# Kernel optimization log

Measured on AMD Instinct MI355X. Metric: run time of the kernel, lower is better.

## Reference

```python
import jax, jax.numpy as jnp
import numpy as np

B, T, D = 2, 2048, 2048
H, HD = 16, 128          # n_heads, head_dim
K, L = 4, 24             # n_bases, total_layers
FF = D * 1               # ff_mult = 1 (required by route_down dim match)


def setup_inputs() -> dict:
    key = jax.random.key(0)
    ks = jax.random.split(key, 16)
    s = jnp.float32(0.02)
    bias_base = jnp.zeros((L, K), jnp.float32).at[:, 0].set(5.0)
    return {
        "x": jax.random.normal(ks[0], (B, T, D), jnp.float32),
        "gamma": jnp.ones((D,), jnp.float32),
        "beta": jnp.zeros((D,), jnp.float32),
        "iter_scale": jnp.ones((), jnp.float32),
        "qkv_bases": jax.random.normal(ks[1], (K, 3 * D, D), jnp.float32) * s,
        "o_bases": jax.random.normal(ks[2], (K, D, D), jnp.float32) * s,
        "gate_bases": jax.random.normal(ks[3], (K, FF, D), jnp.float32) * s,
        "up_bases": jax.random.normal(ks[4], (K, FF, D), jnp.float32) * s,
        "down_bases": jax.random.normal(ks[5], (K, D, FF), jnp.float32) * s,
        "route_qkv": jax.random.normal(ks[6], (L, K, D), jnp.float32) * s,
        "route_o": jax.random.normal(ks[7], (L, K, D), jnp.float32) * s,
        "route_gate": jax.random.normal(ks[8], (L, K, D), jnp.float32) * s,
        "route_up": jax.random.normal(ks[9], (L, K, D), jnp.float32) * s,
        "route_down": jax.random.normal(ks[10], (L, K, FF), jnp.float32) * s,
        "bias_qkv": bias_base + 0.1 * jax.random.normal(ks[11], (L, K), jnp.float32),
        "bias_o": bias_base + 0.1 * jax.random.normal(ks[12], (L, K), jnp.float32),
        "bias_gate": bias_base + 0.1 * jax.random.normal(ks[13], (L, K), jnp.float32),
        "bias_up": bias_base + 0.1 * jax.random.normal(ks[14], (L, K), jnp.float32),
        "bias_down": bias_base + 0.1 * jax.random.normal(ks[15], (L, K), jnp.float32),
        "norm1_w": jnp.ones((D,), jnp.float32),
        "norm2_w": jnp.ones((D,), jnp.float32),
        "layer_idx": 5,
    }


def _rmsnorm(x, w):
    eps = jnp.finfo(x.dtype).eps  # nn.RMSNorm default eps
    return x * jax.lax.rsqrt(jnp.mean(x * x, axis=-1, keepdims=True) + eps) * w


def _mixed_linear(x, bases, route_l, bias_l):
    # route_l: (K, d_in), bias_l: (K,) for this layer
    logits = jnp.einsum('btd,kd->btk', x, route_l) / jnp.sqrt(jnp.float32(D)) + bias_l
    alpha = jax.nn.softmax(logits, axis=-1)                    # (B,T,K)
    y = jnp.einsum('btk,kod,btd->bto', alpha, bases, x)        # weighted combine of K linears
    return y, alpha


def reference(x, gamma, beta, iter_scale, qkv_bases, o_bases, gate_bases, up_bases,
              down_bases, route_qkv, route_o, route_gate, route_up, route_down,
              bias_qkv, bias_o, bias_gate, bias_up, bias_down, norm1_w, norm2_w, layer_idx):
    li = layer_idx
    h = _rmsnorm(x, norm1_w) * gamma + beta
    qkv, a_qkv = _mixed_linear(h, qkv_bases, route_qkv[li], bias_qkv[li])
    qkv = qkv.reshape(B, T, 3, H, HD).transpose(2, 0, 3, 1, 4)  # (3,B,H,T,HD)
    q, k, v = qkv[0], qkv[1], qkv[2]
    scores = jnp.einsum('bhqd,bhkd->bhqk', q, k) / jnp.sqrt(jnp.float32(HD))
    causal = jnp.triu(jnp.ones((T, T), bool), 1)
    scores = jnp.where(causal, -jnp.inf, scores)
    attn = jax.nn.softmax(scores, axis=-1)
    out = jnp.einsum('bhqk,bhkd->bhqd', attn, v).transpose(0, 2, 1, 3).reshape(B, T, D)
    attn_out, _ = _mixed_linear(out, o_bases, route_o[li], bias_o[li])
    x_attn = x + attn_out
    h2 = _rmsnorm(x_attn, norm2_w) * gamma + beta
    gate_out, _ = _mixed_linear(h2, gate_bases, route_gate[li], bias_gate[li])
    up_out, _ = _mixed_linear(h2, up_bases, route_up[li], bias_up[li])
    ffn_in = jax.nn.silu(gate_out) * up_out
    down_out, _ = _mixed_linear(ffn_in, down_bases, route_down[li], bias_down[li])
    x_ffn = x_attn + down_out
    return x + (x_ffn - x) * iter_scale, a_qkv
```

## Files before the change

kernel.cpp:

```cpp
#include <hip/hip_runtime.h>


typedef __attribute__((ext_vector_type(8))) short short8;
typedef __attribute__((ext_vector_type(4))) float f32x4;
typedef __attribute__((ext_vector_type(4))) unsigned uint4_t;

#define BT 4096
#define DD 2048
#define KD 8192
#define NH 16
#define HD_ 128
#define RSCALE 0.02209708691207961f
#define ASCALE 0.08838834764831845f

__device__ inline float bf2f(short s) {
  return __uint_as_float(((unsigned)(unsigned short)s) << 16);
}
__device__ inline short f2bf(float f) {
  unsigned u = __float_as_uint(f);
  u += 0x7FFFu + ((u >> 16) & 1u);
  return (short)(u >> 16);
}
__device__ inline f32x4 zero4() { f32x4 v; v[0]=0.f; v[1]=0.f; v[2]=0.f; v[3]=0.f; return v; }

__device__ inline void async_copy16(const void* g, void* l) {
  __builtin_amdgcn_global_load_lds(
      (const __attribute__((address_space(1))) unsigned*)g,
      (__attribute__((address_space(3))) unsigned*)l, 16, 0, 0);
}

__global__ __launch_bounds__(256)
void cvt_bf16_kernel(const float* __restrict__ in, short* __restrict__ out,
                     const int nchunk) {
  const int i = blockIdx.x * 256 + threadIdx.x;
  if (i >= nchunk) return;
  const float* p = in + (size_t)i * 8;
  float4 u0 = *(const float4*)p;
  float4 u1 = *(const float4*)(p + 4);
  uint4_t pk;
  pk[0] = __builtin_amdgcn_perm(__float_as_uint(u0.y), __float_as_uint(u0.x), 0x07060302);
  pk[1] = __builtin_amdgcn_perm(__float_as_uint(u0.w), __float_as_uint(u0.z), 0x07060302);
  pk[2] = __builtin_amdgcn_perm(__float_as_uint(u1.y), __float_as_uint(u1.x), 0x07060302);
  pk[3] = __builtin_amdgcn_perm(__float_as_uint(u1.w), __float_as_uint(u1.z), 0x07060302);
  *(uint4_t*)(out + (size_t)i * 8) = pk;
}

__global__ __launch_bounds__(256)
void rmsnorm_kernel(const float* __restrict__ x, const float* __restrict__ w,
                    const float* __restrict__ gamma, const float* __restrict__ beta,
                    short* __restrict__ out) {
  const int t = blockIdx.x;
  const float* xr = x + (size_t)t * DD;
  const int base = threadIdx.x * 8;
  float4 v0 = *(const float4*)(xr + base);
  float4 v1 = *(const float4*)(xr + base + 4);
  float ss = v0.x*v0.x + v0.y*v0.y + v0.z*v0.z + v0.w*v0.w
           + v1.x*v1.x + v1.y*v1.y + v1.z*v1.z + v1.w*v1.w;
  #pragma unroll
  for (int off = 32; off > 0; off >>= 1) ss += __shfl_xor(ss, off, 64);
  __shared__ float red[4];
  const int lane = threadIdx.x & 63, wv = threadIdx.x >> 6;
  if (lane == 0) red[wv] = ss;
  __syncthreads();
  const float tot = red[0] + red[1] + red[2] + red[3];
  const float inv = rsqrtf(tot * (1.0f / DD) + 1.1920929e-07f);
  float xv[8] = {v0.x,v0.y,v0.z,v0.w,v1.x,v1.y,v1.z,v1.w};
  short8 o;
  #pragma unroll
  for (int j = 0; j < 8; ++j)
    o[j] = f2bf(xv[j] * inv * w[base+j] * gamma[base+j] + beta[base+j]);
  *(short8*)(out + (size_t)t * DD + base) = o;
}

__global__ __launch_bounds__(64)
void route_kernel(const short* __restrict__ in,
                  const float* __restrict__ routeB,
                  const float* __restrict__ biasB,
                  const int* __restrict__ li_ptr,
                  float* __restrict__ alpha,
                  float* __restrict__ aout)
{
  const int t = blockIdx.x;
  const int lane = threadIdx.x;
  const int li = *li_ptr;
  const float* R = routeB + (size_t)li * 4 * DD;
  const float* bias = biasB + li * 4;
  const short* xr = in + (size_t)t * DD;
  float acc0 = 0.f, acc1 = 0.f, acc2 = 0.f, acc3 = 0.f;
  for (int i = lane; i < DD; i += 64) {
    float v = bf2f(xr[i]);
    acc0 += v * R[i];
    acc1 += v * R[DD + i];
    acc2 += v * R[2*DD + i];
    acc3 += v * R[3*DD + i];
  }
  #pragma unroll
  for (int off = 32; off > 0; off >>= 1) {
    acc0 += __shfl_xor(acc0, off, 64);
    acc1 += __shfl_xor(acc1, off, 64);
    acc2 += __shfl_xor(acc2, off, 64);
    acc3 += __shfl_xor(acc3, off, 64);
  }
  if (lane == 0) {
    float lg[4] = {acc0 * RSCALE + bias[0], acc1 * RSCALE + bias[1],
                   acc2 * RSCALE + bias[2], acc3 * RSCALE + bias[3]};
    float mx = fmaxf(fmaxf(lg[0], lg[1]), fmaxf(lg[2], lg[3]));
    float se = 0.f;
    #pragma unroll
    for (int k = 0; k < 4; ++k) { lg[k] = __expf(lg[k] - mx); se += lg[k]; }
    const float rinv = 1.0f / se;
    #pragma unroll
    for (int k = 0; k < 4; ++k) {
      float a = lg[k] * rinv;
      alpha[(size_t)t*4 + k] = a;
      if (aout) aout[(size_t)t*4 + k] = a;
    }
  }
}

__global__ __launch_bounds__(256)
void expand_kernel(const short* __restrict__ in, const float* __restrict__ alpha,
                   short* __restrict__ out)
{
  const int t = blockIdx.x;
  const short* hr = in + (size_t)t * DD;
  const float a0 = alpha[(size_t)t*4], a1 = alpha[(size_t)t*4+1],
              a2 = alpha[(size_t)t*4+2], a3 = alpha[(size_t)t*4+3];
  const float av[4] = {a0, a1, a2, a3};
  #pragma unroll
  for (int c = 0; c < 4; ++c) {
    int ci = threadIdx.x + 256 * c;
    int kk = ci * 8;
    int kidx = kk >> 11;
    int d = kk & 2047;
    short8 v = *(const short8*)(hr + d);
    float s = av[kidx];
    short8 o;
    #pragma unroll
    for (int j = 0; j < 8; ++j) o[j] = f2bf(bf2f(v[j]) * s);
    *(short8*)(out + (size_t)t * KD + kk) = o;
  }
}

__global__ __launch_bounds__(256)
void gemm_mixed(const short* __restrict__ Aexp,
                const short* __restrict__ Bwb,
                const int N, const int mode,
                const float* __restrict__ xres,
                const float* __restrict__ xattn,
                const float* __restrict__ iter_s,
                void* __restrict__ outp)
{
  __shared__ __align__(16) short As[128*64];
  __shared__ __align__(16) short Bs[128*64];
  const int tid = threadIdx.x;
  const int lane = tid & 63, wave = tid >> 6;
  const int lr = lane & 15, lg = lane >> 4;
  const int wm = (wave & 1) * 64, wn = (wave >> 1) * 64;
  const int m0 = blockIdx.y * 128, n0 = blockIdx.x * 128;

  f32x4 acc[4][4];
  #pragma unroll
  for (int i = 0; i < 4; ++i)
    #pragma unroll
    for (int j = 0; j < 4; ++j) acc[i][j] = zero4();

  const int srow = tid >> 3, sc8 = tid & 7;
  const short* Ab = Aexp + (size_t)(m0 + srow) * KD + sc8 * 8;
  const short* Bb = Bwb + (size_t)(n0 + srow) * DD + sc8 * 8;

  for (int kt = 0; kt < 128; ++kt) {
    const int kk0 = kt << 6;
    const int kidx = kk0 >> 11;
    const int dbase = kk0 & 2047;
    #pragma unroll
    for (int c = 0; c < 4; ++c) {
      const int i = tid + 256 * c;
      async_copy16(Ab + (size_t)(c * 32) * KD + kk0, As + i * 8);
      async_copy16(Bb + ((size_t)kidx * N + c * 32) * DD + dbase, Bs + i * 8);
    }
    __syncthreads();
    #pragma unroll
    for (int s = 0; s < 2; ++s) {
      short8 af[4], bfr[4];
      #pragma unroll
      for (int i = 0; i < 4; ++i) af[i]  = *(const short8*)(As + (wm + i*16 + lr)*64 + s*32 + lg*8);
      #pragma unroll
      for (int j = 0; j < 4; ++j) bfr[j] = *(const short8*)(Bs + (wn + j*16 + lr)*64 + s*32 + lg*8);
      #pragma unroll
      for (int i = 0; i < 4; ++i)
        #pragma unroll
        for (int j = 0; j < 4; ++j)
          acc[i][j] = __builtin_amdgcn_mfma_f32_16x16x32_bf16(af[i], bfr[j], acc[i][j], 0, 0, 0);
    }
    __syncthreads();
  }
  const float is = (mode == 3) ? *iter_s : 0.f;
  #pragma unroll
  for (int i = 0; i < 4; ++i) {
    #pragma unroll
    for (int r = 0; r < 4; ++r) {
      const int m = m0 + wm + i*16 + lg*4 + r;
      #pragma unroll
      for (int j = 0; j < 4; ++j) {
        const int n = n0 + wn + j*16 + lr;
        const float v = acc[i][j][r];
        const size_t idx = (size_t)m * N + n;
        if (mode == 0) {
          ((short*)outp)[idx] = f2bf(v);
        } else if (mode == 2) {
          ((float*)outp)[idx] = xres[idx] + v;
        } else {
          const float xv = xres[idx];
          ((float*)outp)[idx] = xv + (xattn[idx] + v - xv) * is;
        }
      }
    }
  }
}

__global__ __launch_bounds__(256)
void transpose_v_kernel(const short* __restrict__ qkv, short* __restrict__ vt)
{
  __shared__ __align__(16) short tile[64][72];
  const int t0 = blockIdx.x * 64;
  const int hd0 = blockIdx.y * 64;
  const int bh = blockIdx.z;
  const int b = bh >> 4, h = bh & 15;
  const int tid = threadIdx.x;
  #pragma unroll
  for (int c = 0; c < 2; ++c) {
    int ci = tid + 256 * c;
    int tr = ci >> 3, c8 = ci & 7;
    *(short8*)&tile[tr][c8*8] =
      *(const short8*)(qkv + (size_t)(b*2048 + t0 + tr)*6144 + 4096 + h*HD_ + hd0 + c8*8);
  }
  __syncthreads();
  #pragma unroll
  for (int c = 0; c < 2; ++c) {
    int ci = tid + 256 * c;
    int hr = ci >> 3, c8 = ci & 7;
    short8 o;
    #pragma unroll
    for (int j = 0; j < 8; ++j) o[j] = tile[c8*8 + j][hr];
    *(short8*)(vt + (size_t)(bh*HD_ + hd0 + hr)*2048 + t0 + c8*8) = o;
  }
}

__global__ __launch_bounds__(256, 2)
void attn_kernel(const short* __restrict__ qkv,
                 const short* __restrict__ vt,
                 short* __restrict__ attnout)
{
  __shared__ __align__(16) short Ks[32][136];
  __shared__ __align__(16) short Vt[128][40];
  __shared__ __align__(16) short Ps[4][16][40];
  const int bid = blockIdx.x;
  const int qt = bid & 31, bh = bid >> 5;
  const int b = bh >> 4, h = bh & 15;
  const int q0 = qt * 64;
  const int tid = threadIdx.x, lane = tid & 63, w = tid >> 6;
  const int lr = lane & 15, lg = lane >> 4;
  const int q0w = q0 + w * 16;

  short8 qf[4];
  {
    const size_t qbase = (size_t)(b*2048 + q0w + lr) * 6144 + h * HD_;
    #pragma unroll
    for (int s = 0; s < 4; ++s)
      qf[s] = *(const short8*)(qkv + qbase + s*32 + lg*8);
  }
  float m_run[4], l_run[4];
  f32x4 acc[8];
  #pragma unroll
  for (int r = 0; r < 4; ++r) { m_run[r] = -1e30f; l_run[r] = 0.f; }
  #pragma unroll
  for (int dt = 0; dt < 8; ++dt) acc[dt] = zero4();

  const int ntiles = (q0 + 64) >> 5;
  for (int jt = 0; jt < ntiles; ++jt) {
    const int j0 = jt << 5;
    #pragma unroll
    for (int c = 0; c < 2; ++c) {
      int ci = tid + 256 * c;
      int key = ci >> 4, hd8 = ci & 15;
      *(short8*)&Ks[key][hd8*8] =
        *(const short8*)(qkv + (size_t)(b*2048 + j0 + key)*6144 + 2048 + h*HD_ + hd8*8);
    }
    #pragma unroll
    for (int c = 0; c < 2; ++c) {
      int ci = tid + 256 * c;
      int hd = ci >> 2, k8 = ci & 3;
      *(short8*)&Vt[hd][k8*8] =
        *(const short8*)(vt + (size_t)(bh*HD_ + hd)*2048 + j0 + k8*8);
    }
    __syncthreads();
    f32x4 sc0 = zero4(), sc1 = zero4();
    #pragma unroll
    for (int s = 0; s < 4; ++s) {
      short8 kb0 = *(const short8*)&Ks[lr][s*32 + lg*8];
      short8 kb1 = *(const short8*)&Ks[16 + lr][s*32 + lg*8];
      sc0 = __builtin_amdgcn_mfma_f32_16x16x32_bf16(qf[s], kb0, sc0, 0, 0, 0);
      sc1 = __builtin_amdgcn_mfma_f32_16x16x32_bf16(qf[s], kb1, sc1, 0, 0, 0);
    }
    float pv0[4], pv1[4], al[4];
    #pragma unroll
    for (int r = 0; r < 4; ++r) {
      const int q = q0w + lg*4 + r;
      float v0 = sc0[r] * ASCALE; if (j0 + lr > q)      v0 = -1e30f;
      float v1 = sc1[r] * ASCALE; if (j0 + 16 + lr > q) v1 = -1e30f;
      float mx = fmaxf(v0, v1);
      mx = fmaxf(mx, __shfl_xor(mx, 1, 16));
      mx = fmaxf(mx, __shfl_xor(mx, 2, 16));
      mx = fmaxf(mx, __shfl_xor(mx, 4, 16));
      mx = fmaxf(mx, __shfl_xor(mx, 8, 16));
      const float mnew = fmaxf(m_run[r], mx);
      const float a = __expf(m_run[r] - mnew);
      v0 = __expf(v0 - mnew);
      v1 = __expf(v1 - mnew);
      float rs = v0 + v1;
      rs += __shfl_xor(rs, 1, 16);
      rs += __shfl_xor(rs, 2, 16);
      rs += __shfl_xor(rs, 4, 16);
      rs += __shfl_xor(rs, 8, 16);
      l_run[r] = l_run[r] * a + rs;
      m_run[r] = mnew;
      al[r] = a; pv0[r] = v0; pv1[r] = v1;
    }
    #pragma unroll
    for (int dt = 0; dt < 8; ++dt)
      #pragma unroll
      for (int r = 0; r < 4; ++r) acc[dt][r] *= al[r];
    #pragma unroll
    for (int r = 0; r < 4; ++r) {
      Ps[w][lg*4 + r][lr]      = f2bf(pv0[r]);
      Ps[w][lg*4 + r][16 + lr] = f2bf(pv1[r]);
    }
    short8 pa = *(const short8*)&Ps[w][lr][lg*8];
    #pragma unroll
    for (int dt = 0; dt < 8; ++dt) {
      short8 vb = *(const short8*)&Vt[dt*16 + lr][lg*8];
      acc[dt] = __builtin_amdgcn_mfma_f32_16x16x32_bf16(pa, vb, acc[dt], 0, 0, 0);
    }
    __syncthreads();
  }
  #pragma unroll
  for (int dt = 0; dt < 8; ++dt) {
    #pragma unroll
    for (int r = 0; r < 4; ++r) {
      const int q = q0w + lg*4 + r;
      attnout[(size_t)(b*2048 + q)*2048 + h*HD_ + dt*16 + lr] = f2bf(acc[dt][r] / l_run[r]);
    }
  }
}

__global__ __launch_bounds__(256)
void silu_mul_kernel(const short* __restrict__ g, const short* __restrict__ u,
                     short* __restrict__ out)
{
  const int i = blockIdx.x * 256 + threadIdx.x;
  short8 gv = ((const short8*)g)[i];
  short8 uv = ((const short8*)u)[i];
  short8 o;
  #pragma unroll
  for (int j = 0; j < 8; ++j) {
    float xg = bf2f(gv[j]);
    float s = xg / (1.0f + __expf(-xg));
    o[j] = f2bf(s * bf2f(uv[j]));
  }
  ((short8*)out)[i] = o;
}

extern "C" void kernel_launch(void* const* d_in, const int* in_sizes, int n_in,
                              void* d_out, int out_size, void* d_ws, size_t ws_size,
                              hipStream_t stream) {
  const float* x          = (const float*)d_in[0];
  const float* gamma      = (const float*)d_in[1];
  const float* beta       = (const float*)d_in[2];
  const float* iter_scale = (const float*)d_in[3];
  const float* qkv_bases  = (const float*)d_in[4];
  const float* o_bases    = (const float*)d_in[5];
  const float* gate_bases = (const float*)d_in[6];
  const float* up_bases   = (const float*)d_in[7];
  const float* down_bases = (const float*)d_in[8];
  const float* route_qkv  = (const float*)d_in[9];
  const float* route_o    = (const float*)d_in[10];
  const float* route_gate = (const float*)d_in[11];
  const float* route_up   = (const float*)d_in[12];
  const float* route_down = (const float*)d_in[13];
  const float* bias_qkv   = (const float*)d_in[14];
  const float* bias_o     = (const float*)d_in[15];
  const float* bias_gate  = (const float*)d_in[16];
  const float* bias_up    = (const float*)d_in[17];
  const float* bias_down  = (const float*)d_in[18];
  const float* norm1_w    = (const float*)d_in[19];
  const float* norm2_w    = (const float*)d_in[20];
  const int*   li         = (const int*)d_in[21];

  float* out0 = (float*)d_out;
  float* aout = out0 + (size_t)BT * DD;

  char* ws = (char*)d_ws;
  short* hbuf    = (short*)(ws + 0);
  float* alpha   = (float*)(ws + 16777216);
  short* Aexp    = (short*)(ws + 16842752);
  short* Bconv   = (short*)(ws + 83951616);
  short* qkvbuf  = (short*)(ws + 184614912);
  short* vtbuf   = (short*)(ws + 234946560);
  short* attnout = (short*)(ws + 251723776);
  float* x_attn  = (float*)(ws + 184614912);
  short* gatebuf = (short*)(ws + 234946560);
  short* upbuf   = (short*)(ws + 251723776);

  const int NCH_QKV = 50331648 / 8;
  const int NCH_D   = 16777216 / 8;

  rmsnorm_kernel<<<BT, 256, 0, stream>>>(x, norm1_w, gamma, beta, hbuf);
  cvt_bf16_kernel<<<NCH_QKV/256, 256, 0, stream>>>(qkv_bases, Bconv, NCH_QKV);
  route_kernel<<<BT, 64, 0, stream>>>(hbuf, route_qkv, bias_qkv, li, alpha, aout);
  expand_kernel<<<BT, 256, 0, stream>>>(hbuf, alpha, Aexp);
  gemm_mixed<<<dim3(48, 32), 256, 0, stream>>>(Aexp, Bconv, 6144, 0,
                                               nullptr, nullptr, nullptr, qkvbuf);
  transpose_v_kernel<<<dim3(32, 2, 32), 256, 0, stream>>>(qkvbuf, vtbuf);
  attn_kernel<<<1024, 256, 0, stream>>>(qkvbuf, vtbuf, attnout);
  cvt_bf16_kernel<<<NCH_D/256, 256, 0, stream>>>(o_bases, Bconv, NCH_D);
  route_kernel<<<BT, 64, 0, stream>>>(attnout, route_o, bias_o, li, alpha, nullptr);
  expand_kernel<<<BT, 256, 0, stream>>>(attnout, alpha, Aexp);
  gemm_mixed<<<dim3(16, 32), 256, 0, stream>>>(Aexp, Bconv, 2048, 2,
                                               x, nullptr, nullptr, x_attn);
  rmsnorm_kernel<<<BT, 256, 0, stream>>>(x_attn, norm2_w, gamma, beta, hbuf);
  cvt_bf16_kernel<<<NCH_D/256, 256, 0, stream>>>(gate_bases, Bconv, NCH_D);
  route_kernel<<<BT, 64, 0, stream>>>(hbuf, route_gate, bias_gate, li, alpha, nullptr);
  expand_kernel<<<BT, 256, 0, stream>>>(hbuf, alpha, Aexp);
  gemm_mixed<<<dim3(16, 32), 256, 0, stream>>>(Aexp, Bconv, 2048, 0,
                                               nullptr, nullptr, nullptr, gatebuf);
  cvt_bf16_kernel<<<NCH_D/256, 256, 0, stream>>>(up_bases, Bconv, NCH_D);
  route_kernel<<<BT, 64, 0, stream>>>(hbuf, route_up, bias_up, li, alpha, nullptr);
  expand_kernel<<<BT, 256, 0, stream>>>(hbuf, alpha, Aexp);
  gemm_mixed<<<dim3(16, 32), 256, 0, stream>>>(Aexp, Bconv, 2048, 0,
                                               nullptr, nullptr, nullptr, upbuf);
  silu_mul_kernel<<<4096, 256, 0, stream>>>(gatebuf, upbuf, gatebuf);
  cvt_bf16_kernel<<<NCH_D/256, 256, 0, stream>>>(down_bases, Bconv, NCH_D);
  route_kernel<<<BT, 64, 0, stream>>>(gatebuf, route_down, bias_down, li, alpha, nullptr);
  expand_kernel<<<BT, 256, 0, stream>>>(gatebuf, alpha, Aexp);
  gemm_mixed<<<dim3(16, 32), 256, 0, stream>>>(Aexp, Bconv, 2048, 3,
                                               x, x_attn, iter_scale, out0);
}
```

Before: 2.158 ms.

## Split-K the four square mixed GEMMs with a separate reduce-epilogue kernel

```diff
diff --git a/kernel.cpp b/kernel.cpp
--- a/kernel.cpp
+++ b/kernel.cpp
@@ -149,7 +149,8 @@
                 const float* __restrict__ xres,
                 const float* __restrict__ xattn,
                 const float* __restrict__ iter_s,
-                void* __restrict__ outp)
+                void* __restrict__ outp,
+                const int nkt)
 {
   __shared__ __align__(16) short As[128*64];
   __shared__ __align__(16) short Bs[128*64];
@@ -158,6 +159,8 @@
   const int lr = lane & 15, lg = lane >> 4;
   const int wm = (wave & 1) * 64, wn = (wave >> 1) * 64;
   const int m0 = blockIdx.y * 128, n0 = blockIdx.x * 128;
+  const int z = blockIdx.z;
+  const int kt0 = z * nkt;
 
   f32x4 acc[4][4];
   #pragma unroll
@@ -169,7 +172,7 @@
   const short* Ab = Aexp + (size_t)(m0 + srow) * KD + sc8 * 8;
   const short* Bb = Bwb + (size_t)(n0 + srow) * DD + sc8 * 8;
 
-  for (int kt = 0; kt < 128; ++kt) {
+  for (int kt = kt0; kt < kt0 + nkt; ++kt) {
     const int kk0 = kt << 6;
     const int kidx = kk0 >> 11;
     const int dbase = kk0 & 2047;
@@ -196,6 +199,7 @@
     __syncthreads();
   }
   const float is = (mode == 3) ? *iter_s : 0.f;
+  float* Ppart = (mode == 4) ? ((float*)outp + (size_t)z * ((size_t)BT * DD)) : nullptr;
   #pragma unroll
   for (int i = 0; i < 4; ++i) {
     #pragma unroll
@@ -210,12 +214,55 @@
           ((short*)outp)[idx] = f2bf(v);
         } else if (mode == 2) {
           ((float*)outp)[idx] = xres[idx] + v;
-        } else {
+        } else if (mode == 3) {
           const float xv = xres[idx];
           ((float*)outp)[idx] = xv + (xattn[idx] + v - xv) * is;
+        } else {
+          Ppart[idx] = v;
         }
       }
     }
+  }
+}
+
+__global__ __launch_bounds__(256)
+void reduce_split(const float* __restrict__ p,
+                  const float* __restrict__ x,
+                  const float* __restrict__ xattn,
+                  const float* __restrict__ iter_s,
+                  const int mode, void* __restrict__ outp)
+{
+  const size_t i = ((size_t)blockIdx.x * 256 + threadIdx.x) * 8;
+  const float* p1 = p + (size_t)BT * DD;
+  float4 a0 = *(const float4*)(p + i);
+  float4 a1 = *(const float4*)(p + i + 4);
+  float4 b0 = *(const float4*)(p1 + i);
+  float4 b1 = *(const float4*)(p1 + i + 4);
+  float s[8] = {a0.x+b0.x, a0.y+b0.y, a0.z+b0.z, a0.w+b0.w,
+                a1.x+b1.x, a1.y+b1.y, a1.z+b1.z, a1.w+b1.w};
+  if (mode == 0) {
+    short8 o;
+    #pragma unroll
+    for (int j = 0; j < 8; ++j) o[j] = f2bf(s[j]);
+    *(short8*)((short*)outp + i) = o;
+  } else if (mode == 2) {
+    float4 x0 = *(const float4*)(x + i);
+    float4 x1 = *(const float4*)(x + i + 4);
+    float xv[8] = {x0.x,x0.y,x0.z,x0.w,x1.x,x1.y,x1.z,x1.w};
+    float* op = (float*)outp;
+    #pragma unroll
+    for (int j = 0; j < 8; ++j) op[i + j] = xv[j] + s[j];
+  } else {
+    const float is = *iter_s;
+    float4 x0 = *(const float4*)(x + i);
+    float4 x1 = *(const float4*)(x + i + 4);
+    float4 t0 = *(const float4*)(xattn + i);
+    float4 t1 = *(const float4*)(xattn + i + 4);
+    float xv[8] = {x0.x,x0.y,x0.z,x0.w,x1.x,x1.y,x1.z,x1.w};
+    float tv[8] = {t0.x,t0.y,t0.z,t0.w,t1.x,t1.y,t1.z,t1.w};
+    float* op = (float*)outp;
+    #pragma unroll
+    for (int j = 0; j < 8; ++j) op[i + j] = xv[j] + (tv[j] + s[j] - xv[j]) * is;
   }
 }
 
@@ -411,6 +458,7 @@
   float* x_attn  = (float*)(ws + 184614912);
   short* gatebuf = (short*)(ws + 234946560);
   short* upbuf   = (short*)(ws + 251723776);
+  float* part    = (float*)(ws + 117506048);
 
   const int NCH_QKV = 50331648 / 8;
   const int NCH_D   = 16777216 / 8;
@@ -420,29 +468,33 @@
   route_kernel<<<BT, 64, 0, stream>>>(hbuf, route_qkv, bias_qkv, li, alpha, aout);
   expand_kernel<<<BT, 256, 0, stream>>>(hbuf, alpha, Aexp);
   gemm_mixed<<<dim3(48, 32), 256, 0, stream>>>(Aexp, Bconv, 6144, 0,
-                                               nullptr, nullptr, nullptr, qkvbuf);
+                                               nullptr, nullptr, nullptr, qkvbuf, 128);
   transpose_v_kernel<<<dim3(32, 2, 32), 256, 0, stream>>>(qkvbuf, vtbuf);
   attn_kernel<<<1024, 256, 0, stream>>>(qkvbuf, vtbuf, attnout);
   cvt_bf16_kernel<<<NCH_D/256, 256, 0, stream>>>(o_bases, Bconv, NCH_D);
   route_kernel<<<BT, 64, 0, stream>>>(attnout, route_o, bias_o, li, alpha, nullptr);
   expand_kernel<<<BT, 256, 0, stream>>>(attnout, alpha, Aexp);
-  gemm_mixed<<<dim3(16, 32), 256, 0, stream>>>(Aexp, Bconv, 2048, 2,
-                                               x, nullptr, nullptr, x_attn);
+  gemm_mixed<<<dim3(16, 32, 2), 256, 0, stream>>>(Aexp, Bconv, 2048, 4,
+                                                  nullptr, nullptr, nullptr, part, 64);
+  reduce_split<<<4096, 256, 0, stream>>>(part, x, nullptr, nullptr, 2, x_attn);
   rmsnorm_kernel<<<BT, 256, 0, stream>>>(x_attn, norm2_w, gamma, beta, hbuf);
   cvt_bf16_kernel<<<NCH_D/256, 256, 0, stream>>>(gate_bases, Bconv, NCH_D);
   route_kernel<<<BT, 64, 0, stream>>>(hbuf, route_gate, bias_gate, li, alpha, nullptr);
   expand_kernel<<<BT, 256, 0, stream>>>(hbuf, alpha, Aexp);
-  gemm_mixed<<<dim3(16, 32), 256, 0, stream>>>(Aexp, Bconv, 2048, 0,
-                                               nullptr, nullptr, nullptr, gatebuf);
+  gemm_mixed<<<dim3(16, 32, 2), 256, 0, stream>>>(Aexp, Bconv, 2048, 4,
+                                                  nullptr, nullptr, nullptr, part, 64);
+  reduce_split<<<4096, 256, 0, stream>>>(part, nullptr, nullptr, nullptr, 0, gatebuf);
   cvt_bf16_kernel<<<NCH_D/256, 256, 0, stream>>>(up_bases, Bconv, NCH_D);
   route_kernel<<<BT, 64, 0, stream>>>(hbuf, route_up, bias_up, li, alpha, nullptr);
   expand_kernel<<<BT, 256, 0, stream>>>(hbuf, alpha, Aexp);
-  gemm_mixed<<<dim3(16, 32), 256, 0, stream>>>(Aexp, Bconv, 2048, 0,
-                                               nullptr, nullptr, nullptr, upbuf);
+  gemm_mixed<<<dim3(16, 32, 2), 256, 0, stream>>>(Aexp, Bconv, 2048, 4,
+                                                  nullptr, nullptr, nullptr, part, 64);
+  reduce_split<<<4096, 256, 0, stream>>>(part, nullptr, nullptr, nullptr, 0, upbuf);
   silu_mul_kernel<<<4096, 256, 0, stream>>>(gatebuf, upbuf, gatebuf);
   cvt_bf16_kernel<<<NCH_D/256, 256, 0, stream>>>(down_bases, Bconv, NCH_D);
   route_kernel<<<BT, 64, 0, stream>>>(gatebuf, route_down, bias_down, li, alpha, nullptr);
   expand_kernel<<<BT, 256, 0, stream>>>(gatebuf, alpha, Aexp);
-  gemm_mixed<<<dim3(16, 32), 256, 0, stream>>>(Aexp, Bconv, 2048, 3,
-                                               x, x_attn, iter_scale, out0);
-}
+  gemm_mixed<<<dim3(16, 32, 2), 256, 0, stream>>>(Aexp, Bconv, 2048, 4,
+                                                  nullptr, nullptr, nullptr, part, 64);
+  reduce_split<<<4096, 256, 0, stream>>>(part, x, x_attn, iter_scale, 3, out0);
+}
```

Result: slower. 2.310 ms (+7.0%).

## Replace expanded-K mixed GEMMs with wide-N GEMM plus alpha-weighted combine

Applied to the files above, without the earlier changes.

```diff
diff --git a/kernel.cpp b/kernel.cpp
--- a/kernel.cpp
+++ b/kernel.cpp
@@ -143,13 +143,9 @@
 }
 
 __global__ __launch_bounds__(256)
-void gemm_mixed(const short* __restrict__ Aexp,
-                const short* __restrict__ Bwb,
-                const int N, const int mode,
-                const float* __restrict__ xres,
-                const float* __restrict__ xattn,
-                const float* __restrict__ iter_s,
-                void* __restrict__ outp)
+void gemm_qkv(const short* __restrict__ Aexp,
+              const short* __restrict__ Bwb,
+              short* __restrict__ outp)
 {
   __shared__ __align__(16) short As[128*64];
   __shared__ __align__(16) short Bs[128*64];
@@ -177,7 +173,7 @@
     for (int c = 0; c < 4; ++c) {
       const int i = tid + 256 * c;
       async_copy16(Ab + (size_t)(c * 32) * KD + kk0, As + i * 8);
-      async_copy16(Bb + ((size_t)kidx * N + c * 32) * DD + dbase, Bs + i * 8);
+      async_copy16(Bb + ((size_t)kidx * 6144 + c * 32) * DD + dbase, Bs + i * 8);
     }
     __syncthreads();
     #pragma unroll
@@ -195,7 +191,6 @@
     }
     __syncthreads();
   }
-  const float is = (mode == 3) ? *iter_s : 0.f;
   #pragma unroll
   for (int i = 0; i < 4; ++i) {
     #pragma unroll
@@ -204,18 +199,130 @@
       #pragma unroll
       for (int j = 0; j < 4; ++j) {
         const int n = n0 + wn + j*16 + lr;
-        const float v = acc[i][j][r];
-        const size_t idx = (size_t)m * N + n;
-        if (mode == 0) {
-          ((short*)outp)[idx] = f2bf(v);
-        } else if (mode == 2) {
-          ((float*)outp)[idx] = xres[idx] + v;
-        } else {
-          const float xv = xres[idx];
-          ((float*)outp)[idx] = xv + (xattn[idx] + v - xv) * is;
-        }
+        outp[(size_t)m * 6144 + n] = f2bf(acc[i][j][r]);
       }
     }
+  }
+}
+
+__global__ __launch_bounds__(256)
+void gemm_wide(const short* __restrict__ A,
+               const short* __restrict__ Bc,
+               short* __restrict__ Z)
+{
+  __shared__ __align__(16) short As[128*64];
+  __shared__ __align__(16) short Bs[128*64];
+  const int tid = threadIdx.x;
+  const int lane = tid & 63, wave = tid >> 6;
+  const int lr = lane & 15, lg = lane >> 4;
+  const int wm = (wave & 1) * 64, wn = (wave >> 1) * 64;
+  const int m0 = blockIdx.y * 128, n0 = blockIdx.x * 128;
+
+  f32x4 acc[4][4];
+  #pragma unroll
+  for (int i = 0; i < 4; ++i)
+    #pragma unroll
+    for (int j = 0; j < 4; ++j) acc[i][j] = zero4();
+
+  const int srow = tid >> 3, sc8 = tid & 7;
+  const short* Ab = A  + (size_t)(m0 + srow) * DD + sc8 * 8;
+  const short* Bb = Bc + (size_t)(n0 + srow) * DD + sc8 * 8;
+
+  for (int kt = 0; kt < 32; ++kt) {
+    const int kk0 = kt << 6;
+    #pragma unroll
+    for (int c = 0; c < 4; ++c) {
+      const int i = tid + 256 * c;
+      async_copy16(Ab + (size_t)(c * 32) * DD + kk0, As + i * 8);
+      async_copy16(Bb + (size_t)(c * 32) * DD + kk0, Bs + i * 8);
+    }
+    __syncthreads();
+    #pragma unroll
+    for (int s = 0; s < 2; ++s) {
+      short8 af[4], bfr[4];
+      #pragma unroll
+      for (int i = 0; i < 4; ++i) af[i]  = *(const short8*)(As + (wm + i*16 + lr)*64 + s*32 + lg*8);
+      #pragma unroll
+      for (int j = 0; j < 4; ++j) bfr[j] = *(const short8*)(Bs + (wn + j*16 + lr)*64 + s*32 + lg*8);
+      #pragma unroll
+      for (int i = 0; i < 4; ++i)
+        #pragma unroll
+        for (int j = 0; j < 4; ++j)
+          acc[i][j] = __builtin_amdgcn_mfma_f32_16x16x32_bf16(af[i], bfr[j], acc[i][j], 0, 0, 0);
+    }
+    __syncthreads();
+  }
+  #pragma unroll
+  for (int i = 0; i < 4; ++i) {
+    #pragma unroll
+    for (int r = 0; r < 4; ++r) {
+      const int m = m0 + wm + i*16 + lg*4 + r;
+      #pragma unroll
+      for (int j = 0; j < 4; ++j) {
+        const int n = n0 + wn + j*16 + lr;
+        Z[(size_t)m * 8192 + n] = f2bf(acc[i][j][r]);
+      }
+    }
+  }
+}
+
+__global__ __launch_bounds__(256)
+void combine_kernel(const short* __restrict__ Z,
+                    const float* __restrict__ alpha,
+                    const int mode,
+                    const float* __restrict__ x,
+                    const float* __restrict__ xattn,
+                    const float* __restrict__ iter_s,
+                    const short* __restrict__ gate,
+                    void* __restrict__ outp)
+{
+  const int t = blockIdx.x;
+  const int d0 = threadIdx.x * 8;
+  const float a0 = alpha[(size_t)t*4],   a1 = alpha[(size_t)t*4+1],
+              a2 = alpha[(size_t)t*4+2], a3 = alpha[(size_t)t*4+3];
+  const short* zr = Z + (size_t)t * 8192 + d0;
+  short8 z0 = *(const short8*)(zr);
+  short8 z1 = *(const short8*)(zr + 2048);
+  short8 z2 = *(const short8*)(zr + 4096);
+  short8 z3 = *(const short8*)(zr + 6144);
+  float y[8];
+  #pragma unroll
+  for (int j = 0; j < 8; ++j)
+    y[j] = a0*bf2f(z0[j]) + a1*bf2f(z1[j]) + a2*bf2f(z2[j]) + a3*bf2f(z3[j]);
+  const size_t base = (size_t)t * DD + d0;
+  if (mode == 0) {
+    short8 o;
+    #pragma unroll
+    for (int j = 0; j < 8; ++j) o[j] = f2bf(y[j]);
+    *(short8*)((short*)outp + base) = o;
+  } else if (mode == 1) {
+    float4 x0 = *(const float4*)(x + base);
+    float4 x1 = *(const float4*)(x + base + 4);
+    float xv[8] = {x0.x,x0.y,x0.z,x0.w,x1.x,x1.y,x1.z,x1.w};
+    float* op = (float*)outp;
+    #pragma unroll
+    for (int j = 0; j < 8; ++j) op[base + j] = xv[j] + y[j];
+  } else if (mode == 2) {
+    short8 gv = *(const short8*)(gate + base);
+    short8 o;
+    #pragma unroll
+    for (int j = 0; j < 8; ++j) {
+      float xg = bf2f(gv[j]);
+      float s = xg / (1.0f + __expf(-xg));
+      o[j] = f2bf(s * y[j]);
+    }
+    *(short8*)((short*)outp + base) = o;
+  } else {
+    const float is = *iter_s;
+    float4 x0 = *(const float4*)(x + base);
+    float4 x1 = *(const float4*)(x + base + 4);
+    float4 t0 = *(const float4*)(xattn + base);
+    float4 t1 = *(const float4*)(xattn + base + 4);
+    float xv[8] = {x0.x,x0.y,x0.z,x0.w,x1.x,x1.y,x1.z,x1.w};
+    float tv[8] = {t0.x,t0.y,t0.z,t0.w,t1.x,t1.y,t1.z,t1.w};
+    float* op = (float*)outp;
+    #pragma unroll
+    for (int j = 0; j < 8; ++j) op[base + j] = xv[j] + (tv[j] + y[j] - xv[j]) * is;
   }
 }
 
@@ -352,23 +459,6 @@
       attnout[(size_t)(b*2048 + q)*2048 + h*HD_ + dt*16 + lr] = f2bf(acc[dt][r] / l_run[r]);
     }
   }
-}
-
-__global__ __launch_bounds__(256)
-void silu_mul_kernel(const short* __restrict__ g, const short* __restrict__ u,
-                     short* __restrict__ out)
-{
-  const int i = blockIdx.x * 256 + threadIdx.x;
-  short8 gv = ((const short8*)g)[i];
-  short8 uv = ((const short8*)u)[i];
-  short8 o;
-  #pragma unroll
-  for (int j = 0; j < 8; ++j) {
-    float xg = bf2f(gv[j]);
-    float s = xg / (1.0f + __expf(-xg));
-    o[j] = f2bf(s * bf2f(uv[j]));
-  }
-  ((short8*)out)[i] = o;
 }
 
 extern "C" void kernel_launch(void* const* d_in, const int* in_sizes, int n_in,
@@ -403,14 +493,13 @@
   char* ws = (char*)d_ws;
   short* hbuf    = (short*)(ws + 0);
   float* alpha   = (float*)(ws + 16777216);
-  short* Aexp    = (short*)(ws + 16842752);
+  short* Zbuf    = (short*)(ws + 16842752);
   short* Bconv   = (short*)(ws + 83951616);
   short* qkvbuf  = (short*)(ws + 184614912);
   short* vtbuf   = (short*)(ws + 234946560);
   short* attnout = (short*)(ws + 251723776);
   float* x_attn  = (float*)(ws + 184614912);
-  short* gatebuf = (short*)(ws + 234946560);
-  short* upbuf   = (short*)(ws + 251723776);
+  short* gatebuf = (short*)(ws + 218169344);
 
   const int NCH_QKV = 50331648 / 8;
   const int NCH_D   = 16777216 / 8;
@@ -418,31 +507,29 @@
   rmsnorm_kernel<<<BT, 256, 0, stream>>>(x, norm1_w, gamma, beta, hbuf);
   cvt_bf16_kernel<<<NCH_QKV/256, 256, 0, stream>>>(qkv_bases, Bconv, NCH_QKV);
   route_kernel<<<BT, 64, 0, stream>>>(hbuf, route_qkv, bias_qkv, li, alpha, aout);
-  expand_kernel<<<BT, 256, 0, stream>>>(hbuf, alpha, Aexp);
-  gemm_mixed<<<dim3(48, 32), 256, 0, stream>>>(Aexp, Bconv, 6144, 0,
-                                               nullptr, nullptr, nullptr, qkvbuf);
+  expand_kernel<<<BT, 256, 0, stream>>>(hbuf, alpha, Zbuf);
+  gemm_qkv<<<dim3(48, 32), 256, 0, stream>>>(Zbuf, Bconv, qkvbuf);
   transpose_v_kernel<<<dim3(32, 2, 32), 256, 0, stream>>>(qkvbuf, vtbuf);
   attn_kernel<<<1024, 256, 0, stream>>>(qkvbuf, vtbuf, attnout);
   cvt_bf16_kernel<<<NCH_D/256, 256, 0, stream>>>(o_bases, Bconv, NCH_D);
   route_kernel<<<BT, 64, 0, stream>>>(attnout, route_o, bias_o, li, alpha, nullptr);
-  expand_kernel<<<BT, 256, 0, stream>>>(attnout, alpha, Aexp);
-  gemm_mixed<<<dim3(16, 32), 256, 0, stream>>>(Aexp, Bconv, 2048, 2,
-                                               x, nullptr, nullptr, x_attn);
+  gemm_wide<<<dim3(64, 32), 256, 0, stream>>>(attnout, Bconv, Zbuf);
+  combine_kernel<<<BT, 256, 0, stream>>>(Zbuf, alpha, 1, x, nullptr, nullptr,
+                                         nullptr, x_attn);
   rmsnorm_kernel<<<BT, 256, 0, stream>>>(x_attn, norm2_w, gamma, beta, hbuf);
   cvt_bf16_kernel<<<NCH_D/256, 256, 0, stream>>>(gate_bases, Bconv, NCH_D);
   route_kernel<<<BT, 64, 0, stream>>>(hbuf, route_gate, bias_gate, li, alpha, nullptr);
-  expand_kernel<<<BT, 256, 0, stream>>>(hbuf, alpha, Aexp);
-  gemm_mixed<<<dim3(16, 32), 256, 0, stream>>>(Aexp, Bconv, 2048, 0,
-                                               nullptr, nullptr, nullptr, gatebuf);
+  gemm_wide<<<dim3(64, 32), 256, 0, stream>>>(hbuf, Bconv, Zbuf);
+  combine_kernel<<<BT, 256, 0, stream>>>(Zbuf, alpha, 0, nullptr, nullptr, nullptr,
+                                         nullptr, gatebuf);
   cvt_bf16_kernel<<<NCH_D/256, 256, 0, stream>>>(up_bases, Bconv, NCH_D);
   route_kernel<<<BT, 64, 0, stream>>>(hbuf, route_up, bias_up, li, alpha, nullptr);
-  expand_kernel<<<BT, 256, 0, stream>>>(hbuf, alpha, Aexp);
-  gemm_mixed<<<dim3(16, 32), 256, 0, stream>>>(Aexp, Bconv, 2048, 0,
-                                               nullptr, nullptr, nullptr, upbuf);
-  silu_mul_kernel<<<4096, 256, 0, stream>>>(gatebuf, upbuf, gatebuf);
+  gemm_wide<<<dim3(64, 32), 256, 0, stream>>>(hbuf, Bconv, Zbuf);
+  combine_kernel<<<BT, 256, 0, stream>>>(Zbuf, alpha, 2, nullptr, nullptr, nullptr,
+                                         gatebuf, gatebuf);
   cvt_bf16_kernel<<<NCH_D/256, 256, 0, stream>>>(down_bases, Bconv, NCH_D);
   route_kernel<<<BT, 64, 0, stream>>>(gatebuf, route_down, bias_down, li, alpha, nullptr);
-  expand_kernel<<<BT, 256, 0, stream>>>(gatebuf, alpha, Aexp);
-  gemm_mixed<<<dim3(16, 32), 256, 0, stream>>>(Aexp, Bconv, 2048, 3,
-                                               x, x_attn, iter_scale, out0);
-}
+  gemm_wide<<<dim3(64, 32), 256, 0, stream>>>(gatebuf, Bconv, Zbuf);
+  combine_kernel<<<BT, 256, 0, stream>>>(Zbuf, alpha, 3, x, x_attn, iter_scale,
+                                         nullptr, out0);
+}
```

Measured after the change: 1.996 ms. 7.5% less time.
